# Optimization experiments

Measured on AMD Instinct MI355X. Metric: run time of the kernel, lower is better.

## Reference

```python
import jax, jax.numpy as jnp
import numpy as np


def setup_inputs() -> dict:
    key = jax.random.key(0)
    kq, kk, kv, km = jax.random.split(key, 4)
    B, H, S, D = 4, 16, 1024, 64
    return {
        "Q": jax.random.normal(kq, (B, H, S, D), dtype=jnp.float32),
        "K": jax.random.normal(kk, (B, H, S, D), dtype=jnp.float32),
        "V": jax.random.normal(kv, (B, H, S, D), dtype=jnp.float32),
        "attn_mask": jax.random.uniform(km, (B, H, S, S), dtype=jnp.float32),
        "d_k": 64,
    }


def reference(Q, K, V, attn_mask, d_k):
    # scores = Q K^T / sqrt(d_k): [B,H,S,S]
    scale = 1.0 / np.sqrt(d_k).astype(np.float32)
    scores = jnp.einsum("bhsd,bhtd->bhst", Q, K) * scale
    # NOTE: mask applied via matmul with mask^T (not additive) — faithful to source
    scores = jnp.einsum("bhst,bhut->bhsu", scores, attn_mask)
    attn = jax.nn.softmax(scores, axis=-1)
    context = jnp.einsum("bhst,bhtd->bhsd", attn, V)
    return (context, attn)
```

## Files before the change

kernel.cpp:

```cpp
#include <hip/hip_runtime.h>
#include <hip/hip_bf16.h>


#define BH   64
#define S    1024
#define D    64
#define SCALE 0.125f

static __device__ __forceinline__ void fma4(float4& a, float s, const float4& b) {
    a.x = fmaf(s, b.x, a.x);
    a.y = fmaf(s, b.y, a.y);
    a.z = fmaf(s, b.z, a.z);
    a.w = fmaf(s, b.w, a.w);
}

template <bool TRANS_OUT>
__global__ __launch_bounds__(256) void gemm_ab(const float* __restrict__ A,
                                               const float* __restrict__ B,
                                               float* __restrict__ C) {
    const int bh  = blockIdx.y;
    const int u0  = blockIdx.x * 64;
    const int tid = threadIdx.x;
    const int tx  = tid & 15;
    const int ty  = tid >> 4;

    __shared__ float As[64][68];
    __shared__ float Bs[64][64];

    const float* Ab = A + (size_t)bh * S * S;
    const float* Bb = B + (size_t)bh * S * D;

    float4 acc[4];
#pragma unroll
    for (int i = 0; i < 4; i++) acc[i] = make_float4(0.f, 0.f, 0.f, 0.f);

    const int lr = tid >> 4;
    const int lc = (tid & 15) * 4;

    for (int t0 = 0; t0 < S; t0 += 64) {
#pragma unroll
        for (int k = 0; k < 4; k++) {
            float4 va = *(const float4*)&Ab[(size_t)(u0 + lr + 16 * k) * S + t0 + lc];
            *(float4*)&As[lr + 16 * k][lc] = va;
            float4 vb = *(const float4*)&Bb[(size_t)(t0 + lr + 16 * k) * D + lc];
            *(float4*)&Bs[lr + 16 * k][lc] = vb;
        }
        __syncthreads();
#pragma unroll
        for (int tt = 0; tt < 64; tt += 4) {
            float4 b0 = *(const float4*)&Bs[tt + 0][tx * 4];
            float4 b1 = *(const float4*)&Bs[tt + 1][tx * 4];
            float4 b2 = *(const float4*)&Bs[tt + 2][tx * 4];
            float4 b3 = *(const float4*)&Bs[tt + 3][tx * 4];
#pragma unroll
            for (int i = 0; i < 4; i++) {
                float4 a = *(const float4*)&As[ty * 4 + i][tt];
                fma4(acc[i], a.x, b0);
                fma4(acc[i], a.y, b1);
                fma4(acc[i], a.z, b2);
                fma4(acc[i], a.w, b3);
            }
        }
        __syncthreads();
    }

    if (TRANS_OUT) {
        float* Cb = C + (size_t)bh * D * S;
#pragma unroll
        for (int i = 0; i < 4; i++) {
            const int u = u0 + ty * 4 + i;
            Cb[(size_t)(tx * 4 + 0) * S + u] = acc[i].x;
            Cb[(size_t)(tx * 4 + 1) * S + u] = acc[i].y;
            Cb[(size_t)(tx * 4 + 2) * S + u] = acc[i].z;
            Cb[(size_t)(tx * 4 + 3) * S + u] = acc[i].w;
        }
    } else {
        float* Cb = C + (size_t)bh * S * D;
#pragma unroll
        for (int i = 0; i < 4; i++) {
            *(float4*)&Cb[(size_t)(u0 + ty * 4 + i) * D + tx * 4] = acc[i];
        }
    }
}

__global__ __launch_bounds__(256) void logits_softmax(const float* __restrict__ Q,
                                                      const float* __restrict__ M2T,
                                                      float* __restrict__ attn) {
    const int bh  = blockIdx.y;
    const int s0  = blockIdx.x * 16;
    const int tid = threadIdx.x;
    const int w   = tid >> 6;
    const int l   = tid & 63;

    __shared__ float Qs[16][68];
    {
        const int r = tid >> 4;
        const int c = (tid & 15) * 4;
        float4 v = *(const float4*)&Q[((size_t)bh * S + s0 + r) * D + c];
        v.x *= SCALE; v.y *= SCALE; v.z *= SCALE; v.w *= SCALE;
        *(float4*)&Qs[r][c] = v;
    }
    __syncthreads();

    float4 acc[4][4];
#pragma unroll
    for (int r = 0; r < 4; r++)
#pragma unroll
        for (int c = 0; c < 4; c++) acc[r][c] = make_float4(0.f, 0.f, 0.f, 0.f);

    const float* M2b = M2T + (size_t)bh * D * S;

#pragma unroll 4
    for (int d = 0; d < D; d++) {
        const float* row = M2b + (size_t)d * S;
        float4 m0 = *(const float4*)&row[0 * 256 + 4 * l];
        float4 m1 = *(const float4*)&row[1 * 256 + 4 * l];
        float4 m2 = *(const float4*)&row[2 * 256 + 4 * l];
        float4 m3 = *(const float4*)&row[3 * 256 + 4 * l];
        float q0 = Qs[w * 4 + 0][d];
        float q1 = Qs[w * 4 + 1][d];
        float q2 = Qs[w * 4 + 2][d];
        float q3 = Qs[w * 4 + 3][d];
        fma4(acc[0][0], q0, m0); fma4(acc[0][1], q0, m1); fma4(acc[0][2], q0, m2); fma4(acc[0][3], q0, m3);
        fma4(acc[1][0], q1, m0); fma4(acc[1][1], q1, m1); fma4(acc[1][2], q1, m2); fma4(acc[1][3], q1, m3);
        fma4(acc[2][0], q2, m0); fma4(acc[2][1], q2, m1); fma4(acc[2][2], q2, m2); fma4(acc[2][3], q2, m3);
        fma4(acc[3][0], q3, m0); fma4(acc[3][1], q3, m1); fma4(acc[3][2], q3, m2); fma4(acc[3][3], q3, m3);
    }

#pragma unroll
    for (int r = 0; r < 4; r++) {
        const int s = s0 + w * 4 + r;
        float mx = -3.0e38f;
#pragma unroll
        for (int c = 0; c < 4; c++) {
            float4 v = acc[r][c];
            mx = fmaxf(mx, fmaxf(fmaxf(v.x, v.y), fmaxf(v.z, v.w)));
        }
#pragma unroll
        for (int off = 32; off >= 1; off >>= 1) mx = fmaxf(mx, __shfl_xor(mx, off));
        float sum = 0.f;
#pragma unroll
        for (int c = 0; c < 4; c++) {
            float4 v = acc[r][c];
            v.x = __expf(v.x - mx); v.y = __expf(v.y - mx);
            v.z = __expf(v.z - mx); v.w = __expf(v.w - mx);
            acc[r][c] = v;
            sum += v.x + v.y + v.z + v.w;
        }
#pragma unroll
        for (int off = 32; off >= 1; off >>= 1) sum += __shfl_xor(sum, off);
        const float inv = 1.0f / sum;
        float* out = attn + ((size_t)bh * S + s) * S;
#pragma unroll
        for (int c = 0; c < 4; c++) {
            float4 v = acc[r][c];
            v.x *= inv; v.y *= inv; v.z *= inv; v.w *= inv;
            *(float4*)&out[c * 256 + 4 * l] = v;
        }
    }
}

extern "C" void kernel_launch(void* const* d_in, const int* in_sizes, int n_in,
                              void* d_out, int out_size, void* d_ws, size_t ws_size,
                              hipStream_t stream) {
    const float* Q    = (const float*)d_in[0];
    const float* K    = (const float*)d_in[1];
    const float* V    = (const float*)d_in[2];
    const float* mask = (const float*)d_in[3];
    float* context = (float*)d_out;
    float* attn    = (float*)d_out + (size_t)BH * S * D;
    float* M2T     = (float*)d_ws;

    gemm_ab<true><<<dim3(16, BH), 256, 0, stream>>>(mask, K, M2T);
    logits_softmax<<<dim3(64, BH), 256, 0, stream>>>(Q, M2T, attn);
    gemm_ab<false><<<dim3(16, BH), 256, 0, stream>>>(attn, V, context);
}
```

Before: 784.3 us.

## Use split-bf16 MFMA (3-term) for all three GEMMs with pre-split K/V

Replaces the fp32 FMA GEMMs with bf16 MFMA instructions. Each fp32 operand is split into hi and lo bf16 parts and three products (hh, hl, lh) are accumulated to approximate fp32 accuracy. K and V are pre-split and transposed by a new kernel. The mask and attn operands are split on the fly while staging into LDS, with register prefetch of the next tile. The logits/softmax kernel now uses MFMA with a cross-wave max/sum reduction, at the cost of some precision loss versus true fp32.

```diff
diff --git a/kernel.cpp b/kernel.cpp
--- a/kernel.cpp
+++ b/kernel.cpp
@@ -1,163 +1,286 @@
 #include <hip/hip_runtime.h>
-#include <hip/hip_bf16.h>
-
-
-#define BH   64
-#define S    1024
-#define D    64
+
+
+#define S 1024
+#define D 64
+#define BH 64
 #define SCALE 0.125f
 
-static __device__ __forceinline__ void fma4(float4& a, float s, const float4& b) {
-    a.x = fmaf(s, b.x, a.x);
-    a.y = fmaf(s, b.y, a.y);
-    a.z = fmaf(s, b.z, a.z);
-    a.w = fmaf(s, b.w, a.w);
-}
-
-template <bool TRANS_OUT>
-__global__ __launch_bounds__(256) void gemm_ab(const float* __restrict__ A,
-                                               const float* __restrict__ B,
-                                               float* __restrict__ C) {
-    const int bh  = blockIdx.y;
-    const int u0  = blockIdx.x * 64;
-    const int tid = threadIdx.x;
-    const int tx  = tid & 15;
-    const int ty  = tid >> 4;
-
-    __shared__ float As[64][68];
-    __shared__ float Bs[64][64];
-
-    const float* Ab = A + (size_t)bh * S * S;
-    const float* Bb = B + (size_t)bh * S * D;
-
-    float4 acc[4];
-#pragma unroll
-    for (int i = 0; i < 4; i++) acc[i] = make_float4(0.f, 0.f, 0.f, 0.f);
-
-    const int lr = tid >> 4;
-    const int lc = (tid & 15) * 4;
-
-    for (int t0 = 0; t0 < S; t0 += 64) {
-#pragma unroll
-        for (int k = 0; k < 4; k++) {
-            float4 va = *(const float4*)&Ab[(size_t)(u0 + lr + 16 * k) * S + t0 + lc];
-            *(float4*)&As[lr + 16 * k][lc] = va;
-            float4 vb = *(const float4*)&Bb[(size_t)(t0 + lr + 16 * k) * D + lc];
-            *(float4*)&Bs[lr + 16 * k][lc] = vb;
-        }
+typedef short s16x8 __attribute__((ext_vector_type(8)));
+typedef float f32x4 __attribute__((ext_vector_type(4)));
+typedef unsigned short u16;
+
+__device__ __forceinline__ void split2(float x, u16& h, u16& l) {
+    unsigned u = __float_as_uint(x);
+    h = (u16)(u >> 16);
+    float xh = __uint_as_float(u & 0xFFFF0000u);
+    l = (u16)(__float_as_uint(x - xh) >> 16);
+}
+
+__global__ __launch_bounds__(256) void split_transpose(
+        const float* __restrict__ Kin, const float* __restrict__ Vin,
+        u16* __restrict__ Khi, u16* __restrict__ Klo,
+        u16* __restrict__ Vhi, u16* __restrict__ Vlo) {
+    const float* X = blockIdx.z ? Vin : Kin;
+    u16* Xhi = blockIdx.z ? Vhi : Khi;
+    u16* Xlo = blockIdx.z ? Vlo : Klo;
+    const int bh = blockIdx.y, t0 = blockIdx.x * 64, tid = threadIdx.x;
+    __shared__ u16 Th[64 * 72], Tl[64 * 72];
+    {
+        const int tr = tid >> 2, ds = (tid & 3) * 16;
+        const float* src = X + ((size_t)bh * S + t0 + tr) * D + ds;
+        u16 h[16], l[16];
+#pragma unroll
+        for (int j = 0; j < 4; j++) {
+            float4 v = *(const float4*)(src + j * 4);
+            split2(v.x, h[4 * j + 0], l[4 * j + 0]);
+            split2(v.y, h[4 * j + 1], l[4 * j + 1]);
+            split2(v.z, h[4 * j + 2], l[4 * j + 2]);
+            split2(v.w, h[4 * j + 3], l[4 * j + 3]);
+        }
+#pragma unroll
+        for (int hf = 0; hf < 2; hf++) {
+            uint4 ph, pl;
+            ph.x = h[8*hf+0] | ((unsigned)h[8*hf+1] << 16);
+            ph.y = h[8*hf+2] | ((unsigned)h[8*hf+3] << 16);
+            ph.z = h[8*hf+4] | ((unsigned)h[8*hf+5] << 16);
+            ph.w = h[8*hf+6] | ((unsigned)h[8*hf+7] << 16);
+            pl.x = l[8*hf+0] | ((unsigned)l[8*hf+1] << 16);
+            pl.y = l[8*hf+2] | ((unsigned)l[8*hf+3] << 16);
+            pl.z = l[8*hf+4] | ((unsigned)l[8*hf+5] << 16);
+            pl.w = l[8*hf+6] | ((unsigned)l[8*hf+7] << 16);
+            *(uint4*)&Th[tr * 72 + ds + hf * 8] = ph;
+            *(uint4*)&Tl[tr * 72 + ds + hf * 8] = pl;
+        }
+    }
+    __syncthreads();
+    {
+        const int d = tid >> 2, ts = (tid & 3) * 16;
+        u16 h[16], l[16];
+#pragma unroll
+        for (int j = 0; j < 16; j++) {
+            h[j] = Th[(ts + j) * 72 + d];
+            l[j] = Tl[(ts + j) * 72 + d];
+        }
+        u16* oh = Xhi + ((size_t)bh * D + d) * S + t0 + ts;
+        u16* ol = Xlo + ((size_t)bh * D + d) * S + t0 + ts;
+#pragma unroll
+        for (int hf = 0; hf < 2; hf++) {
+            uint4 ph, pl;
+            ph.x = h[8*hf+0] | ((unsigned)h[8*hf+1] << 16);
+            ph.y = h[8*hf+2] | ((unsigned)h[8*hf+3] << 16);
+            ph.z = h[8*hf+4] | ((unsigned)h[8*hf+5] << 16);
+            ph.w = h[8*hf+6] | ((unsigned)h[8*hf+7] << 16);
+            pl.x = l[8*hf+0] | ((unsigned)l[8*hf+1] << 16);
+            pl.y = l[8*hf+2] | ((unsigned)l[8*hf+3] << 16);
+            pl.z = l[8*hf+4] | ((unsigned)l[8*hf+5] << 16);
+            pl.w = l[8*hf+6] | ((unsigned)l[8*hf+7] << 16);
+            *(uint4*)(oh + hf * 8) = ph;
+            *(uint4*)(ol + hf * 8) = pl;
+        }
+    }
+}
+
+template <bool SPLIT_OUT>
+__global__ __launch_bounds__(256) void gemm_split(
+        const float* __restrict__ A, const u16* __restrict__ Bhg,
+        const u16* __restrict__ Blg, float* __restrict__ Cf,
+        u16* __restrict__ Ch, u16* __restrict__ Cl) {
+    const int bh = blockIdx.y, mblk = blockIdx.x * 128, tid = threadIdx.x;
+    const int lane = tid & 63, wave = tid >> 6;
+    const int q = lane >> 4, r = lane & 15;
+    const int wy = wave >> 1, wx = wave & 1;
+
+    __shared__ u16 Ah[128 * 72], Al[128 * 72];
+    __shared__ u16 Bsh[64 * 72], Bsl[64 * 72];
+
+    const float* Ab = A + (size_t)bh * S * S + (size_t)mblk * S;
+    const u16* Bhb = Bhg + (size_t)bh * D * S;
+    const u16* Blb = Blg + (size_t)bh * D * S;
+
+    f32x4 acc[4][2];
+#pragma unroll
+    for (int mt = 0; mt < 4; mt++)
+#pragma unroll
+        for (int nt = 0; nt < 2; nt++) acc[mt][nt] = 0.0f;
+
+    const int arow = tid >> 3, aseg = tid & 7;
+    const int brow = tid >> 2, bseg = tid & 3;
+
+    float4 pa[4][2];
+    uint4 pbh[2], pbl[2];
+
+    auto prefetch = [&](int k0) {
+#pragma unroll
+        for (int i = 0; i < 4; i++) {
+            const float* p = Ab + (size_t)(arow + 32 * i) * S + k0 + aseg * 8;
+            pa[i][0] = *(const float4*)p;
+            pa[i][1] = *(const float4*)(p + 4);
+        }
+        const u16* ph = Bhb + (size_t)brow * S + k0 + bseg * 16;
+        const u16* pl = Blb + (size_t)brow * S + k0 + bseg * 16;
+        pbh[0] = *(const uint4*)ph; pbh[1] = *(const uint4*)(ph + 8);
+        pbl[0] = *(const uint4*)pl; pbl[1] = *(const uint4*)(pl + 8);
+    };
+
+    prefetch(0);
+    for (int t = 0; t < 16; t++) {
+        if (t) __syncthreads();
+#pragma unroll
+        for (int i = 0; i < 4; i++) {
+            u16 h[8], l[8];
+            float* pv = (float*)&pa[i][0];
+#pragma unroll
+            for (int j = 0; j < 8; j++) split2(pv[j], h[j], l[j]);
+            uint4 ph, pl;
+            ph.x = h[0] | ((unsigned)h[1] << 16); ph.y = h[2] | ((unsigned)h[3] << 16);
+            ph.z = h[4] | ((unsigned)h[5] << 16); ph.w = h[6] | ((unsigned)h[7] << 16);
+            pl.x = l[0] | ((unsigned)l[1] << 16); pl.y = l[2] | ((unsigned)l[3] << 16);
+            pl.z = l[4] | ((unsigned)l[5] << 16); pl.w = l[6] | ((unsigned)l[7] << 16);
+            *(uint4*)&Ah[(arow + 32 * i) * 72 + aseg * 8] = ph;
+            *(uint4*)&Al[(arow + 32 * i) * 72 + aseg * 8] = pl;
+        }
+        *(uint4*)&Bsh[brow * 72 + bseg * 16]     = pbh[0];
+        *(uint4*)&Bsh[brow * 72 + bseg * 16 + 8] = pbh[1];
+        *(uint4*)&Bsl[brow * 72 + bseg * 16]     = pbl[0];
+        *(uint4*)&Bsl[brow * 72 + bseg * 16 + 8] = pbl[1];
         __syncthreads();
-#pragma unroll
-        for (int tt = 0; tt < 64; tt += 4) {
-            float4 b0 = *(const float4*)&Bs[tt + 0][tx * 4];
-            float4 b1 = *(const float4*)&Bs[tt + 1][tx * 4];
-            float4 b2 = *(const float4*)&Bs[tt + 2][tx * 4];
-            float4 b3 = *(const float4*)&Bs[tt + 3][tx * 4];
+        if (t < 15) prefetch((t + 1) * 64);
+#pragma unroll
+        for (int kk = 0; kk < 2; kk++) {
+            s16x8 afh[4], afl[4], bfh[2], bfl[2];
+#pragma unroll
+            for (int mt = 0; mt < 4; mt++) {
+                const int row = wy * 64 + mt * 16 + r;
+                afh[mt] = *(const s16x8*)&Ah[row * 72 + kk * 32 + q * 8];
+                afl[mt] = *(const s16x8*)&Al[row * 72 + kk * 32 + q * 8];
+            }
+#pragma unroll
+            for (int nt = 0; nt < 2; nt++) {
+                const int col = wx * 32 + nt * 16 + r;
+                bfh[nt] = *(const s16x8*)&Bsh[col * 72 + kk * 32 + q * 8];
+                bfl[nt] = *(const s16x8*)&Bsl[col * 72 + kk * 32 + q * 8];
+            }
+#pragma unroll
+            for (int mt = 0; mt < 4; mt++)
+#pragma unroll
+                for (int nt = 0; nt < 2; nt++) {
+                    acc[mt][nt] = __builtin_amdgcn_mfma_f32_16x16x32_bf16(afh[mt], bfh[nt], acc[mt][nt], 0, 0, 0);
+                    acc[mt][nt] = __builtin_amdgcn_mfma_f32_16x16x32_bf16(afh[mt], bfl[nt], acc[mt][nt], 0, 0, 0);
+                    acc[mt][nt] = __builtin_amdgcn_mfma_f32_16x16x32_bf16(afl[mt], bfh[nt], acc[mt][nt], 0, 0, 0);
+                }
+        }
+    }
+#pragma unroll
+    for (int mt = 0; mt < 4; mt++)
+#pragma unroll
+        for (int nt = 0; nt < 2; nt++)
 #pragma unroll
             for (int i = 0; i < 4; i++) {
-                float4 a = *(const float4*)&As[ty * 4 + i][tt];
-                fma4(acc[i], a.x, b0);
-                fma4(acc[i], a.y, b1);
-                fma4(acc[i], a.z, b2);
-                fma4(acc[i], a.w, b3);
+                const int m = mblk + wy * 64 + mt * 16 + q * 4 + i;
+                const int n = wx * 32 + nt * 16 + r;
+                const float v = acc[mt][nt][i];
+                if (SPLIT_OUT) {
+                    u16 h, l;
+                    split2(v, h, l);
+                    Ch[((size_t)bh * S + m) * D + n] = h;
+                    Cl[((size_t)bh * S + m) * D + n] = l;
+                } else {
+                    Cf[((size_t)bh * S + m) * D + n] = v;
+                }
             }
-        }
-        __syncthreads();
-    }
-
-    if (TRANS_OUT) {
-        float* Cb = C + (size_t)bh * D * S;
+}
+
+__global__ __launch_bounds__(256) void logits_softmax_mfma(
+        const float* __restrict__ Q, const u16* __restrict__ M2h,
+        const u16* __restrict__ M2l, float* __restrict__ attn) {
+    const int bh = blockIdx.y, s0 = blockIdx.x * 16, tid = threadIdx.x;
+    const int w = tid >> 6, lane = tid & 63, q = lane >> 4, r = lane & 15;
+    __shared__ u16 Qh[16 * 72], Ql[16 * 72];
+    __shared__ float Lmx[4][16], Lsm[4][16];
+    {
+        const int row = tid >> 4, c4 = (tid & 15) * 4;
+        float4 v = *(const float4*)&Q[((size_t)bh * S + s0 + row) * D + c4];
+        u16 h[4], l[4];
+        split2(v.x * SCALE, h[0], l[0]);
+        split2(v.y * SCALE, h[1], l[1]);
+        split2(v.z * SCALE, h[2], l[2]);
+        split2(v.w * SCALE, h[3], l[3]);
+        uint2 ph, pl;
+        ph.x = h[0] | ((unsigned)h[1] << 16); ph.y = h[2] | ((unsigned)h[3] << 16);
+        pl.x = l[0] | ((unsigned)l[1] << 16); pl.y = l[2] | ((unsigned)l[3] << 16);
+        *(uint2*)&Qh[row * 72 + c4] = ph;
+        *(uint2*)&Ql[row * 72 + c4] = pl;
+    }
+    __syncthreads();
+    s16x8 aq[2][2];
+#pragma unroll
+    for (int kk = 0; kk < 2; kk++) {
+        aq[kk][0] = *(const s16x8*)&Qh[r * 72 + kk * 32 + q * 8];
+        aq[kk][1] = *(const s16x8*)&Ql[r * 72 + kk * 32 + q * 8];
+    }
+    f32x4 acc[16];
+#pragma unroll
+    for (int nt = 0; nt < 16; nt++) acc[nt] = 0.0f;
+    const u16* Bh = M2h + (size_t)bh * S * D;
+    const u16* Bl = M2l + (size_t)bh * S * D;
+#pragma unroll 4
+    for (int nt = 0; nt < 16; nt++) {
+        const int u = w * 256 + nt * 16 + r;
+#pragma unroll
+        for (int kk = 0; kk < 2; kk++) {
+            s16x8 bh8 = *(const s16x8*)&Bh[(size_t)u * D + kk * 32 + q * 8];
+            s16x8 bl8 = *(const s16x8*)&Bl[(size_t)u * D + kk * 32 + q * 8];
+            acc[nt] = __builtin_amdgcn_mfma_f32_16x16x32_bf16(aq[kk][0], bh8, acc[nt], 0, 0, 0);
+            acc[nt] = __builtin_amdgcn_mfma_f32_16x16x32_bf16(aq[kk][0], bl8, acc[nt], 0, 0, 0);
+            acc[nt] = __builtin_amdgcn_mfma_f32_16x16x32_bf16(aq[kk][1], bh8, acc[nt], 0, 0, 0);
+        }
+    }
+    float lmax[4], lsum[4];
+#pragma unroll
+    for (int i = 0; i < 4; i++) {
+        float m = -3.0e38f;
+#pragma unroll
+        for (int nt = 0; nt < 16; nt++) m = fmaxf(m, acc[nt][i]);
+#pragma unroll
+        for (int off = 8; off >= 1; off >>= 1) m = fmaxf(m, __shfl_xor(m, off));
+        lmax[i] = m;
+        float s = 0.f;
+#pragma unroll
+        for (int nt = 0; nt < 16; nt++) {
+            float e = __expf(acc[nt][i] - m);
+            acc[nt][i] = e;
+            s += e;
+        }
+#pragma unroll
+        for (int off = 8; off >= 1; off >>= 1) s += __shfl_xor(s, off);
+        lsum[i] = s;
+    }
+    if (r == 0) {
 #pragma unroll
         for (int i = 0; i < 4; i++) {
-            const int u = u0 + ty * 4 + i;
-            Cb[(size_t)(tx * 4 + 0) * S + u] = acc[i].x;
-            Cb[(size_t)(tx * 4 + 1) * S + u] = acc[i].y;
-            Cb[(size_t)(tx * 4 + 2) * S + u] = acc[i].z;
-            Cb[(size_t)(tx * 4 + 3) * S + u] = acc[i].w;
-        }
-    } else {
-        float* Cb = C + (size_t)bh * S * D;
-#pragma unroll
-        for (int i = 0; i < 4; i++) {
-            *(float4*)&Cb[(size_t)(u0 + ty * 4 + i) * D + tx * 4] = acc[i];
-        }
-    }
-}
-
-__global__ __launch_bounds__(256) void logits_softmax(const float* __restrict__ Q,
-                                                      const float* __restrict__ M2T,
-                                                      float* __restrict__ attn) {
-    const int bh  = blockIdx.y;
-    const int s0  = blockIdx.x * 16;
-    const int tid = threadIdx.x;
-    const int w   = tid >> 6;
-    const int l   = tid & 63;
-
-    __shared__ float Qs[16][68];
-    {
-        const int r = tid >> 4;
-        const int c = (tid & 15) * 4;
-        float4 v = *(const float4*)&Q[((size_t)bh * S + s0 + r) * D + c];
-        v.x *= SCALE; v.y *= SCALE; v.z *= SCALE; v.w *= SCALE;
-        *(float4*)&Qs[r][c] = v;
+            Lmx[w][q * 4 + i] = lmax[i];
+            Lsm[w][q * 4 + i] = lsum[i];
+        }
     }
     __syncthreads();
-
-    float4 acc[4][4];
-#pragma unroll
-    for (int r = 0; r < 4; r++)
-#pragma unroll
-        for (int c = 0; c < 4; c++) acc[r][c] = make_float4(0.f, 0.f, 0.f, 0.f);
-
-    const float* M2b = M2T + (size_t)bh * D * S;
-
-#pragma unroll 4
-    for (int d = 0; d < D; d++) {
-        const float* row = M2b + (size_t)d * S;
-        float4 m0 = *(const float4*)&row[0 * 256 + 4 * l];
-        float4 m1 = *(const float4*)&row[1 * 256 + 4 * l];
-        float4 m2 = *(const float4*)&row[2 * 256 + 4 * l];
-        float4 m3 = *(const float4*)&row[3 * 256 + 4 * l];
-        float q0 = Qs[w * 4 + 0][d];
-        float q1 = Qs[w * 4 + 1][d];
-        float q2 = Qs[w * 4 + 2][d];
-        float q3 = Qs[w * 4 + 3][d];
-        fma4(acc[0][0], q0, m0); fma4(acc[0][1], q0, m1); fma4(acc[0][2], q0, m2); fma4(acc[0][3], q0, m3);
-        fma4(acc[1][0], q1, m0); fma4(acc[1][1], q1, m1); fma4(acc[1][2], q1, m2); fma4(acc[1][3], q1, m3);
-        fma4(acc[2][0], q2, m0); fma4(acc[2][1], q2, m1); fma4(acc[2][2], q2, m2); fma4(acc[2][3], q2, m3);
-        fma4(acc[3][0], q3, m0); fma4(acc[3][1], q3, m1); fma4(acc[3][2], q3, m2); fma4(acc[3][3], q3, m3);
-    }
-
-#pragma unroll
-    for (int r = 0; r < 4; r++) {
-        const int s = s0 + w * 4 + r;
-        float mx = -3.0e38f;
-#pragma unroll
-        for (int c = 0; c < 4; c++) {
-            float4 v = acc[r][c];
-            mx = fmaxf(mx, fmaxf(fmaxf(v.x, v.y), fmaxf(v.z, v.w)));
-        }
-#pragma unroll
-        for (int off = 32; off >= 1; off >>= 1) mx = fmaxf(mx, __shfl_xor(mx, off));
-        float sum = 0.f;
-#pragma unroll
-        for (int c = 0; c < 4; c++) {
-            float4 v = acc[r][c];
-            v.x = __expf(v.x - mx); v.y = __expf(v.y - mx);
-            v.z = __expf(v.z - mx); v.w = __expf(v.w - mx);
-            acc[r][c] = v;
-            sum += v.x + v.y + v.z + v.w;
-        }
-#pragma unroll
-        for (int off = 32; off >= 1; off >>= 1) sum += __shfl_xor(sum, off);
-        const float inv = 1.0f / sum;
-        float* out = attn + ((size_t)bh * S + s) * S;
-#pragma unroll
-        for (int c = 0; c < 4; c++) {
-            float4 v = acc[r][c];
-            v.x *= inv; v.y *= inv; v.z *= inv; v.w *= inv;
-            *(float4*)&out[c * 256 + 4 * l] = v;
-        }
-    }
+    float scl[4];
+#pragma unroll
+    for (int i = 0; i < 4; i++) {
+        const int row = q * 4 + i;
+        float gmax = fmaxf(fmaxf(Lmx[0][row], Lmx[1][row]), fmaxf(Lmx[2][row], Lmx[3][row]));
+        float gsum = Lsm[0][row] * __expf(Lmx[0][row] - gmax)
+                   + Lsm[1][row] * __expf(Lmx[1][row] - gmax)
+                   + Lsm[2][row] * __expf(Lmx[2][row] - gmax)
+                   + Lsm[3][row] * __expf(Lmx[3][row] - gmax);
+        scl[i] = __expf(lmax[i] - gmax) / gsum;
+    }
+    float* out = attn + ((size_t)bh * S + s0) * S;
+#pragma unroll
+    for (int nt = 0; nt < 16; nt++)
+#pragma unroll
+        for (int i = 0; i < 4; i++)
+            out[(size_t)(q * 4 + i) * S + w * 256 + nt * 16 + r] = acc[nt][i] * scl[i];
 }
 
 extern "C" void kernel_launch(void* const* d_in, const int* in_sizes, int n_in,
@@ -169,9 +292,17 @@
     const float* mask = (const float*)d_in[3];
     float* context = (float*)d_out;
     float* attn    = (float*)d_out + (size_t)BH * S * D;
-    float* M2T     = (float*)d_ws;
-
-    gemm_ab<true><<<dim3(16, BH), 256, 0, stream>>>(mask, K, M2T);
-    logits_softmax<<<dim3(64, BH), 256, 0, stream>>>(Q, M2T, attn);
-    gemm_ab<false><<<dim3(16, BH), 256, 0, stream>>>(attn, V, context);
-}
+
+    const size_t N = (size_t)BH * S * D;
+    u16* M2h = (u16*)d_ws;
+    u16* M2l = M2h + N;
+    u16* Khi = M2l + N;
+    u16* Klo = Khi + N;
+    u16* Vhi = Klo + N;
+    u16* Vlo = Vhi + N;
+
+    split_transpose<<<dim3(16, BH, 2), 256, 0, stream>>>(K, V, Khi, Klo, Vhi, Vlo);
+    gemm_split<true><<<dim3(8, BH), 256, 0, stream>>>(mask, Khi, Klo, nullptr, M2h, M2l);
+    logits_softmax_mfma<<<dim3(64, BH), 256, 0, stream>>>(Q, M2h, M2l, attn);
+    gemm_split<false><<<dim3(8, BH), 256, 0, stream>>>(attn, Vhi, Vlo, context, nullptr, nullptr);
+}
```

New measurement: 963.6 us. 22.9% more time.
